# Optimization experiments

Hardware: AMD Instinct MI355X
Metric: run time of the kernel (lower is better)

Reference implementation:

```python
import jax, jax.numpy as jnp
import numpy as np

EMBED_DIM = 2048
NUM_HEADS = 16
NUM_KV_HEADS = 4
KEY_DIM = EMBED_DIM // NUM_HEADS  # 128
B, S = 2, 2048


def setup_inputs() -> dict:
    key = jax.random.key(0)
    ks = jax.random.split(key, 8)
    kv_dim = KEY_DIM * NUM_KV_HEADS
    sc_in = 1.0 / np.sqrt(EMBED_DIM)
    return {
        "query": jax.random.normal(ks[0], (B, S, EMBED_DIM), jnp.float32),
        "key": jax.random.normal(ks[1], (B, S, EMBED_DIM), jnp.float32),
        "value": jax.random.normal(ks[2], (B, S, EMBED_DIM), jnp.float32),
        "mask": jnp.ones((B, S), jnp.float32),
        "Wq": jax.random.normal(ks[3], (EMBED_DIM, EMBED_DIM), jnp.float32) * sc_in,
        "Wk": jax.random.normal(ks[4], (EMBED_DIM, kv_dim), jnp.float32) * sc_in,
        "Wv": jax.random.normal(ks[5], (EMBED_DIM, kv_dim), jnp.float32) * sc_in,
        "Wo": jax.random.normal(ks[6], (EMBED_DIM, EMBED_DIM), jnp.float32) * sc_in,
    }


def reference(query, key, value, mask, Wq, Wk, Wv, Wo):
    b, sq, _ = query.shape
    skv = key.shape[1]
    scale = 1.0 / float(KEY_DIM) ** 0.5
    # projections (no bias)
    q = (query @ Wq).reshape(b, sq, NUM_HEADS, KEY_DIM).transpose(0, 2, 1, 3)      # [B,H,Sq,D]
    k = (key @ Wk).reshape(b, skv, NUM_KV_HEADS, KEY_DIM).transpose(0, 2, 1, 3)    # [B,Hkv,Skv,D]
    v = (value @ Wv).reshape(b, skv, NUM_KV_HEADS, KEY_DIM).transpose(0, 2, 1, 3)  # [B,Hkv,Skv,D]
    n_rep = NUM_HEADS // NUM_KV_HEADS
    k_rep = jnp.repeat(k, n_rep, axis=1)  # [B,H,Skv,D]
    v_rep = jnp.repeat(v, n_rep, axis=1)  # [B,H,Skv,D]
    scores = jnp.einsum("bhqd,bhkd->bhqk", q, k_rep) * scale  # [B,H,Sq,Skv]
    scores = scores + (1.0 - mask[:, None, None, :].astype(scores.dtype)) * -1e9
    attn = jax.nn.softmax(scores, axis=-1)
    out = jnp.einsum("bhqk,bhkd->bhqd", attn, v_rep)  # [B,H,Sq,D]
    out = out.transpose(0, 2, 1, 3).reshape(b, sq, EMBED_DIM)
    return out @ Wo
```

## Files before the change

### kernel.cpp

```cpp
#include <hip/hip_runtime.h>
#include <hip/hip_bf16.h>

#define B_    2
#define S_    2048
#define E_    2048
#define H_    16
#define HKV_  4
#define D_    128
#define NTOK  4096
#define KVDIM 512

typedef __bf16 bf16x8 __attribute__((ext_vector_type(8)));
typedef __bf16 bf16x4 __attribute__((ext_vector_type(4)));
typedef float  f32x4  __attribute__((ext_vector_type(4)));

__device__ __forceinline__ void async_copy16(const void* g, void* l) {
  __builtin_amdgcn_global_load_lds(
      (const __attribute__((address_space(1))) unsigned int*)g,
      (__attribute__((address_space(3))) unsigned int*)l, 16, 0, 0);
}

__global__ __launch_bounds__(256) void transpose_all(
    const float* __restrict__ Wq, const float* __restrict__ Wk,
    const float* __restrict__ Wv, const float* __restrict__ Wo,
    __bf16* __restrict__ WTq, __bf16* __restrict__ WTk,
    __bf16* __restrict__ WTv, __bf16* __restrict__ WoT) {
  const float* in;
  __bf16* out;
  int C;
  switch (blockIdx.z) {
    case 0:  in = Wq; out = WTq; C = E_;   break;
    case 1:  in = Wk; out = WTk; C = KVDIM; break;
    case 2:  in = Wv; out = WTv; C = KVDIM; break;
    default: in = Wo; out = WoT; C = E_;   break;
  }
  const int c0 = blockIdx.x * 32;
  if (c0 >= C) return;
  const int r0 = blockIdx.y * 32;
  __shared__ float t[32][33];
  const int tr = threadIdx.x >> 3;
  const int tc = (threadIdx.x & 7) * 4;
  const float* ip = in + (size_t)(r0 + tr) * C + c0 + tc;
#pragma unroll
  for (int i = 0; i < 4; ++i) t[tr][tc + i] = ip[i];
  __syncthreads();
  __bf16* op = out + (size_t)(c0 + tr) * E_ + r0 + tc;
#pragma unroll
  for (int i = 0; i < 4; ++i) op[i] = (__bf16)t[tc + i][tr];
}

__global__ __launch_bounds__(256, 2) void gemm_qkv(
    const float* __restrict__ query, const float* __restrict__ key,
    const float* __restrict__ value, const __bf16* __restrict__ WTq,
    const __bf16* __restrict__ WTk, const __bf16* __restrict__ WTv,
    __bf16* __restrict__ Qp, __bf16* __restrict__ Kp,
    __bf16* __restrict__ Vt) {
  __shared__ __align__(16) __bf16 As[128 * 32];
  __shared__ __align__(16) __bf16 Bs[128 * 32];

  const int bx = blockIdx.x;
  const float* A;
  const __bf16* Bt;
  int n0, N, epi;
  if (bx < 16)      { A = query; Bt = WTq; n0 = bx * 128;        N = E_;    epi = 0; }
  else if (bx < 20) { A = key;   Bt = WTk; n0 = (bx - 16) * 128; N = KVDIM; epi = 0; }
  else              { A = value; Bt = WTv; n0 = (bx - 20) * 128; N = KVDIM; epi = 1; }
  const int m0 = blockIdx.y * 128;
  const int K = E_;

  const int tid = threadIdx.x;
  const int w = tid >> 6;
  const int lane = tid & 63;
  const int quad = lane >> 4;
  const int l16 = lane & 15;
  const int wr = w >> 1, wc = w & 1;
  const int brow = lane >> 2;
  const int bcol = (lane & 3) * 8;
  const int arow = lane >> 2;
  const int acol = (lane & 3) * 8;

  f32x4 acc[4][4] = {};

  for (int k0 = 0; k0 < K; k0 += 32) {
    __syncthreads();
#pragma unroll
    for (int c = 0; c < 2; ++c) {
      const int chunk = w * 2 + c;
      const int row = chunk * 16 + brow;
      async_copy16(Bt + (size_t)(n0 + row) * K + k0 + bcol, &Bs[chunk * 512]);
    }
#pragma unroll
    for (int s = 0; s < 2; ++s) {
      const int row = w * 32 + s * 16 + arow;
      const float* src = A + (size_t)(m0 + row) * K + k0 + acol;
      const f32x4 a0 = *(const f32x4*)src;
      const f32x4 a1 = *(const f32x4*)(src + 4);
      bf16x8 v;
#pragma unroll
      for (int j = 0; j < 4; ++j) { v[j] = (__bf16)a0[j]; v[4 + j] = (__bf16)a1[j]; }
      *(bf16x8*)&As[row * 32 + acol] = v;
    }
    __syncthreads();
    bf16x8 af[4], bfr[4];
#pragma unroll
    for (int i = 0; i < 4; ++i)
      af[i] = *(const bf16x8*)&As[(wr * 64 + i * 16 + l16) * 32 + quad * 8];
#pragma unroll
    for (int j = 0; j < 4; ++j)
      bfr[j] = *(const bf16x8*)&Bs[(wc * 64 + j * 16 + l16) * 32 + quad * 8];
#pragma unroll
    for (int i = 0; i < 4; ++i)
#pragma unroll
      for (int j = 0; j < 4; ++j)
        acc[i][j] = __builtin_amdgcn_mfma_f32_16x16x32_bf16(af[i], bfr[j],
                                                            acc[i][j], 0, 0, 0);
  }

#pragma unroll
  for (int i = 0; i < 4; ++i) {
#pragma unroll
    for (int j = 0; j < 4; ++j) {
#pragma unroll
      for (int r = 0; r < 4; ++r) {
        const int m = m0 + wr * 64 + i * 16 + quad * 4 + r;
        const int n = n0 + wc * 64 + j * 16 + l16;
        if (epi == 0) {
          __bf16* C = (bx < 16) ? Qp : Kp;
          C[(size_t)m * N + n] = (__bf16)acc[i][j][r];
        } else {
          const int b = m >> 11, s = m & (S_ - 1);
          Vt[((size_t)((b * HKV_ + (n >> 7)) * D_ + (n & (D_ - 1)))) * S_ + s] =
              (__bf16)acc[i][j][r];
        }
      }
    }
  }
}

__global__ __launch_bounds__(256, 2) void gemm_o(
    const __bf16* __restrict__ A, const __bf16* __restrict__ Bt,
    float* __restrict__ Cout, int M, int N, int K) {
  __shared__ __align__(16) __bf16 As[128 * 32];
  __shared__ __align__(16) __bf16 Bs[128 * 32];
  const int m0 = blockIdx.y * 128;
  const int n0 = blockIdx.x * 128;
  const int tid = threadIdx.x;
  const int w = tid >> 6;
  const int lane = tid & 63;
  const int quad = lane >> 4;
  const int l16 = lane & 15;
  const int wr = w >> 1, wc = w & 1;
  const int arow = lane >> 2;
  const int acol = (lane & 3) * 8;

  f32x4 acc[4][4] = {};

  for (int k0 = 0; k0 < K; k0 += 32) {
    __syncthreads();
#pragma unroll
    for (int c = 0; c < 2; ++c) {
      const int chunk = w * 2 + c;
      const int row = chunk * 16 + arow;
      async_copy16(A + (size_t)(m0 + row) * K + k0 + acol, &As[chunk * 512]);
      async_copy16(Bt + (size_t)(n0 + row) * K + k0 + acol, &Bs[chunk * 512]);
    }
    __syncthreads();
    bf16x8 af[4], bfr[4];
#pragma unroll
    for (int i = 0; i < 4; ++i)
      af[i] = *(const bf16x8*)&As[(wr * 64 + i * 16 + l16) * 32 + quad * 8];
#pragma unroll
    for (int j = 0; j < 4; ++j)
      bfr[j] = *(const bf16x8*)&Bs[(wc * 64 + j * 16 + l16) * 32 + quad * 8];
#pragma unroll
    for (int i = 0; i < 4; ++i)
#pragma unroll
      for (int j = 0; j < 4; ++j)
        acc[i][j] = __builtin_amdgcn_mfma_f32_16x16x32_bf16(af[i], bfr[j],
                                                            acc[i][j], 0, 0, 0);
  }

#pragma unroll
  for (int i = 0; i < 4; ++i)
#pragma unroll
    for (int j = 0; j < 4; ++j)
#pragma unroll
      for (int r = 0; r < 4; ++r) {
        const int m = m0 + wr * 64 + i * 16 + quad * 4 + r;
        const int n = n0 + wc * 64 + j * 16 + l16;
        Cout[(size_t)m * N + n] = acc[i][j][r];
      }
}

__global__ __launch_bounds__(256, 2) void attn_kernel(
    const __bf16* __restrict__ Q, const __bf16* __restrict__ Kp,
    const __bf16* __restrict__ Vt, const float* __restrict__ mask,
    __bf16* __restrict__ Oa) {
  __shared__ __align__(16) __bf16 K_lds[64][136];
  __shared__ __align__(16) __bf16 V_lds[128][72];
  __shared__ __align__(16) __bf16 P_lds[4][32][72];

  const int tid = threadIdx.x;
  const int w = tid >> 6, lane = tid & 63, quad = lane >> 4, l16 = lane & 15;
  const int bh = blockIdx.y;
  const int b = bh >> 4, h = bh & 15, hkv = h >> 2;
  const int q0 = blockIdx.x * 128 + w * 32;

  const __bf16* qbase = Q + (size_t)(b * S_ + q0) * E_ + h * D_;
  bf16x8 qf[2][4];
#pragma unroll
  for (int m = 0; m < 2; ++m)
#pragma unroll
    for (int ks = 0; ks < 4; ++ks)
      qf[m][ks] = *(const bf16x8*)(qbase + (size_t)(m * 16 + l16) * E_ +
                                   ks * 32 + quad * 8);

  const __bf16* kbase = Kp + (size_t)(b * S_) * KVDIM + hkv * D_;
  const __bf16* vbase = Vt + (size_t)((b * HKV_ + hkv) * D_) * S_;
  const float* mbase = mask + b * S_;

  f32x4 o[2][8] = {};
  f32x4 lsum[2] = {};
  const float scale = 0.08838834764831845f;

  for (int kt = 0; kt < S_; kt += 64) {
    __syncthreads();
#pragma unroll
    for (int i = 0; i < 4; ++i) {
      const int r = w * 16 + i * 4 + (lane >> 4);
      bf16x8 kv = *(const bf16x8*)(kbase + (size_t)(kt + r) * KVDIM +
                                   (lane & 15) * 8);
      *(bf16x8*)&K_lds[r][(lane & 15) * 8] = kv;
    }
#pragma unroll
    for (int i = 0; i < 4; ++i) {
      const int r = w * 32 + i * 8 + (lane >> 3);
      bf16x8 vv = *(const bf16x8*)(vbase + (size_t)r * S_ + kt +
                                   (lane & 7) * 8);
      *(bf16x8*)&V_lds[r][(lane & 7) * 8] = vv;
    }
    __syncthreads();

    f32x4 s[2][4] = {};
#pragma unroll
    for (int ks = 0; ks < 4; ++ks) {
#pragma unroll
      for (int n = 0; n < 4; ++n) {
        bf16x8 kf = *(const bf16x8*)&K_lds[n * 16 + l16][ks * 32 + quad * 8];
        s[0][n] = __builtin_amdgcn_mfma_f32_16x16x32_bf16(qf[0][ks], kf,
                                                          s[0][n], 0, 0, 0);
        s[1][n] = __builtin_amdgcn_mfma_f32_16x16x32_bf16(qf[1][ks], kf,
                                                          s[1][n], 0, 0, 0);
      }
    }

    float bias[4];
#pragma unroll
    for (int n = 0; n < 4; ++n)
      bias[n] = (1.0f - mbase[kt + n * 16 + l16]) * -1e9f;
#pragma unroll
    for (int m = 0; m < 2; ++m) {
#pragma unroll
      for (int n = 0; n < 4; ++n) {
#pragma unroll
        for (int r = 0; r < 4; ++r) {
          const float p = __expf(s[m][n][r] * scale + bias[n]);
          lsum[m][r] += p;
          P_lds[w][m * 16 + quad * 4 + r][n * 16 + l16] = (__bf16)p;
        }
      }
    }

#pragma unroll
    for (int ks2 = 0; ks2 < 2; ++ks2) {
      bf16x8 pa[2];
#pragma unroll
      for (int m = 0; m < 2; ++m)
        pa[m] = *(const bf16x8*)&P_lds[w][m * 16 + l16][ks2 * 32 + quad * 8];
#pragma unroll
      for (int dt = 0; dt < 8; ++dt) {
        bf16x8 vf = *(const bf16x8*)&V_lds[dt * 16 + l16][ks2 * 32 + quad * 8];
        o[0][dt] = __builtin_amdgcn_mfma_f32_16x16x32_bf16(pa[0], vf,
                                                           o[0][dt], 0, 0, 0);
        o[1][dt] = __builtin_amdgcn_mfma_f32_16x16x32_bf16(pa[1], vf,
                                                           o[1][dt], 0, 0, 0);
      }
    }
  }

  __bf16* obase = Oa + (size_t)(b * S_ + q0) * E_ + h * D_;
#pragma unroll
  for (int m = 0; m < 2; ++m) {
#pragma unroll
    for (int r = 0; r < 4; ++r) {
      float v = lsum[m][r];
#pragma unroll
      for (int off = 1; off < 16; off <<= 1) v += __shfl_xor(v, off);
      const float inv = 1.0f / v;
#pragma unroll
      for (int dt = 0; dt < 8; ++dt)
        obase[(size_t)(m * 16 + quad * 4 + r) * E_ + dt * 16 + l16] =
            (__bf16)(o[m][dt][r] * inv);
    }
  }
}

extern "C" void kernel_launch(void* const* d_in, const int* in_sizes, int n_in,
                              void* d_out, int out_size, void* d_ws,
                              size_t ws_size, hipStream_t stream) {
  const float* query = (const float*)d_in[0];
  const float* key   = (const float*)d_in[1];
  const float* value = (const float*)d_in[2];
  const float* mask  = (const float*)d_in[3];
  const float* Wq    = (const float*)d_in[4];
  const float* Wk    = (const float*)d_in[5];
  const float* Wv    = (const float*)d_in[6];
  const float* Wo    = (const float*)d_in[7];
  float* out = (float*)d_out;

  __bf16* ws   = (__bf16*)d_ws;
  __bf16* Qp   = ws;
  __bf16* Kp   = Qp + (size_t)NTOK * E_;
  __bf16* Vt   = Kp + (size_t)NTOK * KVDIM;
  __bf16* WoT  = Vt + (size_t)NTOK * KVDIM;
  __bf16* WTq  = WoT + (size_t)E_ * E_;
  __bf16* WTk  = WTq + (size_t)E_ * E_;
  __bf16* WTv  = WTk + (size_t)KVDIM * E_;
  __bf16* Attn = WTq;

  transpose_all<<<dim3(64, 64, 4), 256, 0, stream>>>(Wq, Wk, Wv, Wo,
                                                     WTq, WTk, WTv, WoT);
  gemm_qkv<<<dim3(24, 32), 256, 0, stream>>>(query, key, value,
                                             WTq, WTk, WTv, Qp, Kp, Vt);
  attn_kernel<<<dim3(S_ / 128, B_ * H_), 256, 0, stream>>>(Qp, Kp, Vt, mask,
                                                           Attn);
  gemm_o<<<dim3(E_ / 128, NTOK / 128), 256, 0, stream>>>(Attn, WoT, out,
                                                         NTOK, E_, E_);
}
```

Before: 404.8 us.

## Add double-buffered swizzled GEMM for Q and O projections, prequantize query

Adds a 512-thread GEMM kernel with a 128x256 tile, a K-step of 64, double-buffered async global-to-LDS loads, an XOR-swizzled LDS layout and raised wave priority around the MFMA blocks. It is used for the Q projection and the output projection. The query is converted to bf16 beforehand in a separate kernel, reusing the output buffer as scratch. K/V projections stay on the old kernel, and the attention kernel gets setprio hints around its MFMA sections. The goal is to hide global load latency and reduce LDS bank conflicts in the large GEMMs, at the cost of an extra conversion pass and higher register/LDS use per block.

```diff
diff --git a/kernel.cpp b/kernel.cpp
--- a/kernel.cpp
+++ b/kernel.cpp
@@ -49,24 +49,140 @@
   for (int i = 0; i < 4; ++i) op[i] = (__bf16)t[tc + i][tr];
 }
 
-__global__ __launch_bounds__(256, 2) void gemm_qkv(
-    const float* __restrict__ query, const float* __restrict__ key,
-    const float* __restrict__ value, const __bf16* __restrict__ WTq,
+__global__ __launch_bounds__(256) void convert_q(const float* __restrict__ in,
+                                                 __bf16* __restrict__ ob) {
+  const size_t i = ((size_t)blockIdx.x * 256 + threadIdx.x) * 8;
+  const f32x4 a0 = *(const f32x4*)(in + i);
+  const f32x4 a1 = *(const f32x4*)(in + i + 4);
+  bf16x8 v;
+#pragma unroll
+  for (int j = 0; j < 4; ++j) { v[j] = (__bf16)a0[j]; v[4 + j] = (__bf16)a1[j]; }
+  *(bf16x8*)(ob + i) = v;
+}
+
+__global__ __launch_bounds__(512, 1) void gemm_pipe(
+    const __bf16* __restrict__ A, const __bf16* __restrict__ Bt,
+    float* __restrict__ Cf, __bf16* __restrict__ Cb, int M, int N, int K,
+    int epi) {
+  __shared__ __align__(16) __bf16 lds[2 * 24576];
+
+  const int n0 = blockIdx.x * 256;
+  const int m0 = blockIdx.y * 128;
+  const int tid = threadIdx.x;
+  const int w = tid >> 6;
+  const int lane = tid & 63;
+  const int quad = lane >> 4;
+  const int l16 = lane & 15;
+  const int wm = w >> 2;
+  const int wn = w & 3;
+  const int lr = lane >> 3;
+  const int ls = lane & 7;
+
+  const __bf16* pa[2];
+  const __bf16* pb[4];
+#pragma unroll
+  for (int r = 0; r < 2; ++r) {
+    const int row = r * 64 + w * 8 + lr;
+    pa[r] = A + (size_t)(m0 + row) * K + ((ls ^ (row & 7)) * 8);
+  }
+#pragma unroll
+  for (int r = 0; r < 4; ++r) {
+    const int row = r * 64 + w * 8 + lr;
+    pb[r] = Bt + (size_t)(n0 + row) * K + ((ls ^ (row & 7)) * 8);
+  }
+
+  auto stage = [&](int bufi) {
+    __bf16* base = lds + bufi * 24576;
+#pragma unroll
+    for (int r = 0; r < 2; ++r) {
+      async_copy16(pa[r], base + (size_t)(r * 64 + w * 8) * 64);
+      pa[r] += 64;
+    }
+#pragma unroll
+    for (int r = 0; r < 4; ++r) {
+      async_copy16(pb[r], base + 8192 + (size_t)(r * 64 + w * 8) * 64);
+      pb[r] += 64;
+    }
+  };
+
+  f32x4 acc[4][4] = {};
+  const int NT = K >> 6;
+  const int xr = l16 & 7;
+
+  stage(0);
+  stage(1);
+
+  for (int t = 0; t < NT; ++t) {
+    if (t < NT - 1) {
+      asm volatile("s_waitcnt vmcnt(6)\n\ts_barrier" ::: "memory");
+    } else {
+      asm volatile("s_waitcnt vmcnt(0)\n\ts_barrier" ::: "memory");
+    }
+    const __bf16* lA = lds + (t & 1) * 24576;
+    const __bf16* lB = lA + 8192;
+
+    bf16x8 af[4][2], bfr[4][2];
+#pragma unroll
+    for (int f = 0; f < 4; ++f) {
+      const int rowb = (wm * 64 + f * 16 + l16) * 64;
+#pragma unroll
+      for (int ks = 0; ks < 2; ++ks)
+        af[f][ks] = *(const bf16x8*)&lA[rowb + (((ks * 4 + quad) ^ xr) * 8)];
+    }
+#pragma unroll
+    for (int g = 0; g < 4; ++g) {
+      const int rowb = (wn * 64 + g * 16 + l16) * 64;
+#pragma unroll
+      for (int ks = 0; ks < 2; ++ks)
+        bfr[g][ks] = *(const bf16x8*)&lB[rowb + (((ks * 4 + quad) ^ xr) * 8)];
+    }
+    asm volatile("s_waitcnt lgkmcnt(0)\n\ts_barrier" ::: "memory");
+    if (t + 2 < NT) stage(t & 1);
+
+    __builtin_amdgcn_s_setprio(1);
+#pragma unroll
+    for (int f = 0; f < 4; ++f)
+#pragma unroll
+      for (int g = 0; g < 4; ++g) {
+        acc[f][g] = __builtin_amdgcn_mfma_f32_16x16x32_bf16(af[f][0], bfr[g][0],
+                                                            acc[f][g], 0, 0, 0);
+        acc[f][g] = __builtin_amdgcn_mfma_f32_16x16x32_bf16(af[f][1], bfr[g][1],
+                                                            acc[f][g], 0, 0, 0);
+      }
+    __builtin_amdgcn_s_setprio(0);
+  }
+
+#pragma unroll
+  for (int f = 0; f < 4; ++f) {
+#pragma unroll
+    for (int g = 0; g < 4; ++g) {
+#pragma unroll
+      for (int r = 0; r < 4; ++r) {
+        const int m = m0 + wm * 64 + f * 16 + quad * 4 + r;
+        const int n = n0 + wn * 64 + g * 16 + l16;
+        if (epi == 0) Cf[(size_t)m * N + n] = acc[f][g][r];
+        else          Cb[(size_t)m * N + n] = (__bf16)acc[f][g][r];
+      }
+    }
+  }
+}
+
+__global__ __launch_bounds__(256, 2) void gemm_kv(
+    const float* __restrict__ key, const float* __restrict__ value,
     const __bf16* __restrict__ WTk, const __bf16* __restrict__ WTv,
-    __bf16* __restrict__ Qp, __bf16* __restrict__ Kp,
-    __bf16* __restrict__ Vt) {
+    __bf16* __restrict__ Kp, __bf16* __restrict__ Vt) {
   __shared__ __align__(16) __bf16 As[128 * 32];
   __shared__ __align__(16) __bf16 Bs[128 * 32];
 
   const int bx = blockIdx.x;
   const float* A;
   const __bf16* Bt;
-  int n0, N, epi;
-  if (bx < 16)      { A = query; Bt = WTq; n0 = bx * 128;        N = E_;    epi = 0; }
-  else if (bx < 20) { A = key;   Bt = WTk; n0 = (bx - 16) * 128; N = KVDIM; epi = 0; }
-  else              { A = value; Bt = WTv; n0 = (bx - 20) * 128; N = KVDIM; epi = 1; }
+  int n0, epi;
+  if (bx < 4) { A = key;   Bt = WTk; n0 = bx * 128;       epi = 0; }
+  else        { A = value; Bt = WTv; n0 = (bx - 4) * 128; epi = 1; }
   const int m0 = blockIdx.y * 128;
   const int K = E_;
+  const int N = KVDIM;
 
   const int tid = threadIdx.x;
   const int w = tid >> 6;
@@ -125,8 +241,7 @@
         const int m = m0 + wr * 64 + i * 16 + quad * 4 + r;
         const int n = n0 + wc * 64 + j * 16 + l16;
         if (epi == 0) {
-          __bf16* C = (bx < 16) ? Qp : Kp;
-          C[(size_t)m * N + n] = (__bf16)acc[i][j][r];
+          Kp[(size_t)m * N + n] = (__bf16)acc[i][j][r];
         } else {
           const int b = m >> 11, s = m & (S_ - 1);
           Vt[((size_t)((b * HKV_ + (n >> 7)) * D_ + (n & (D_ - 1)))) * S_ + s] =
@@ -135,61 +250,6 @@
       }
     }
   }
-}
-
-__global__ __launch_bounds__(256, 2) void gemm_o(
-    const __bf16* __restrict__ A, const __bf16* __restrict__ Bt,
-    float* __restrict__ Cout, int M, int N, int K) {
-  __shared__ __align__(16) __bf16 As[128 * 32];
-  __shared__ __align__(16) __bf16 Bs[128 * 32];
-  const int m0 = blockIdx.y * 128;
-  const int n0 = blockIdx.x * 128;
-  const int tid = threadIdx.x;
-  const int w = tid >> 6;
-  const int lane = tid & 63;
-  const int quad = lane >> 4;
-  const int l16 = lane & 15;
-  const int wr = w >> 1, wc = w & 1;
-  const int arow = lane >> 2;
-  const int acol = (lane & 3) * 8;
-
-  f32x4 acc[4][4] = {};
-
-  for (int k0 = 0; k0 < K; k0 += 32) {
-    __syncthreads();
-#pragma unroll
-    for (int c = 0; c < 2; ++c) {
-      const int chunk = w * 2 + c;
-      const int row = chunk * 16 + arow;
-      async_copy16(A + (size_t)(m0 + row) * K + k0 + acol, &As[chunk * 512]);
-      async_copy16(Bt + (size_t)(n0 + row) * K + k0 + acol, &Bs[chunk * 512]);
-    }
-    __syncthreads();
-    bf16x8 af[4], bfr[4];
-#pragma unroll
-    for (int i = 0; i < 4; ++i)
-      af[i] = *(const bf16x8*)&As[(wr * 64 + i * 16 + l16) * 32 + quad * 8];
-#pragma unroll
-    for (int j = 0; j < 4; ++j)
-      bfr[j] = *(const bf16x8*)&Bs[(wc * 64 + j * 16 + l16) * 32 + quad * 8];
-#pragma unroll
-    for (int i = 0; i < 4; ++i)
-#pragma unroll
-      for (int j = 0; j < 4; ++j)
-        acc[i][j] = __builtin_amdgcn_mfma_f32_16x16x32_bf16(af[i], bfr[j],
-                                                            acc[i][j], 0, 0, 0);
-  }
-
-#pragma unroll
-  for (int i = 0; i < 4; ++i)
-#pragma unroll
-    for (int j = 0; j < 4; ++j)
-#pragma unroll
-      for (int r = 0; r < 4; ++r) {
-        const int m = m0 + wr * 64 + i * 16 + quad * 4 + r;
-        const int n = n0 + wc * 64 + j * 16 + l16;
-        Cout[(size_t)m * N + n] = acc[i][j][r];
-      }
 }
 
 __global__ __launch_bounds__(256, 2) void attn_kernel(
@@ -242,6 +302,7 @@
     __syncthreads();
 
     f32x4 s[2][4] = {};
+    __builtin_amdgcn_s_setprio(1);
 #pragma unroll
     for (int ks = 0; ks < 4; ++ks) {
 #pragma unroll
@@ -253,6 +314,7 @@
                                                           s[1][n], 0, 0, 0);
       }
     }
+    __builtin_amdgcn_s_setprio(0);
 
     float bias[4];
 #pragma unroll
@@ -271,6 +333,7 @@
       }
     }
 
+    __builtin_amdgcn_s_setprio(1);
 #pragma unroll
     for (int ks2 = 0; ks2 < 2; ++ks2) {
       bf16x8 pa[2];
@@ -286,6 +349,7 @@
                                                            o[1][dt], 0, 0, 0);
       }
     }
+    __builtin_amdgcn_s_setprio(0);
   }
 
   __bf16* obase = Oa + (size_t)(b * S_ + q0) * E_ + h * D_;
@@ -327,13 +391,16 @@
   __bf16* WTk  = WTq + (size_t)E_ * E_;
   __bf16* WTv  = WTk + (size_t)KVDIM * E_;
   __bf16* Attn = WTq;
+  __bf16* qb   = (__bf16*)d_out;
 
   transpose_all<<<dim3(64, 64, 4), 256, 0, stream>>>(Wq, Wk, Wv, Wo,
                                                      WTq, WTk, WTv, WoT);
-  gemm_qkv<<<dim3(24, 32), 256, 0, stream>>>(query, key, value,
-                                             WTq, WTk, WTv, Qp, Kp, Vt);
+  convert_q<<<dim3(4096), 256, 0, stream>>>(query, qb);
+  gemm_kv<<<dim3(8, 32), 256, 0, stream>>>(key, value, WTk, WTv, Kp, Vt);
+  gemm_pipe<<<dim3(E_ / 256, NTOK / 128), 512, 0, stream>>>(
+      qb, WTq, nullptr, Qp, NTOK, E_, E_, 1);
   attn_kernel<<<dim3(S_ / 128, B_ * H_), 256, 0, stream>>>(Qp, Kp, Vt, mask,
                                                            Attn);
-  gemm_o<<<dim3(E_ / 128, NTOK / 128), 256, 0, stream>>>(Attn, WoT, out,
-                                                         NTOK, E_, E_);
-}
+  gemm_pipe<<<dim3(E_ / 256, NTOK / 128), 512, 0, stream>>>(
+      Attn, WoT, out, nullptr, NTOK, E_, E_, 0);
+}
```

Measured after the change: 409.2 us. Within noise of the previous version (+1.1%).
